# Kernel optimization log

Measured on AMD Instinct MI355X. Metric: run time of the kernel, lower is better.

## Reference

```python
import jax, jax.numpy as jnp
import numpy as np

B, N, DIM = 16, 1024, 512
H, DH = 8, 64
INNER = H * DH            # 512
FF = 4 * DIM              # 2048
CIN = 2 * DIM             # conv inner dim = dim*expansion_factor = 1024
K = 31                    # depthwise kernel size
MAXPOS = 512
EPS = 1e-5


def layernorm(x, g, b):
    mu = jnp.mean(x, axis=-1, keepdims=True)
    var = jnp.mean(jnp.square(x - mu), axis=-1, keepdims=True)
    return (x - mu) * jax.lax.rsqrt(var + EPS) * g + b


def swish(x):
    return x * jax.nn.sigmoid(x)


def feed_forward(x, w1, b1, w2, b2):
    h = swish(x @ w1 + b1)
    return h @ w2 + b2


def setup_inputs() -> dict:
    key = jax.random.key(0)
    ks = jax.random.split(key, 16)
    s = 0.02
    w = lambda k, shape: (jax.random.normal(k, shape, jnp.float32) * s)
    inp = {
        "x": jax.random.normal(ks[0], (B, N, DIM), jnp.float32),
        # FF1
        "ff1_ln_g": jnp.ones((DIM,), jnp.float32), "ff1_ln_b": jnp.zeros((DIM,), jnp.float32),
        "ff1_w1": w(ks[1], (DIM, FF)), "ff1_b1": jnp.zeros((FF,), jnp.float32),
        "ff1_w2": w(ks[2], (FF, DIM)), "ff1_b2": jnp.zeros((DIM,), jnp.float32),
        # Attention (PreNorm)
        "attn_ln_g": jnp.ones((DIM,), jnp.float32), "attn_ln_b": jnp.zeros((DIM,), jnp.float32),
        "wq": w(ks[3], (DIM, INNER)),
        "wkv": w(ks[4], (DIM, 2 * INNER)),
        "wo": w(ks[5], (INNER, DIM)), "bo": jnp.zeros((DIM,), jnp.float32),
        "rel_emb": w(ks[6], (2 * MAXPOS + 1, DH)),
        # Conv module
        "conv_ln_g": jnp.ones((DIM,), jnp.float32), "conv_ln_b": jnp.zeros((DIM,), jnp.float32),
        "conv1_w": w(ks[7], (DIM, 2 * CIN)), "conv1_b": jnp.zeros((2 * CIN,), jnp.float32),
        "dw_w": w(ks[8], (CIN, 1, K)), "dw_b": jnp.zeros((CIN,), jnp.float32),
        "conv2_w": w(ks[9], (CIN, DIM)), "conv2_b": jnp.zeros((DIM,), jnp.float32),
        # FF2
        "ff2_ln_g": jnp.ones((DIM,), jnp.float32), "ff2_ln_b": jnp.zeros((DIM,), jnp.float32),
        "ff2_w1": w(ks[10], (DIM, FF)), "ff2_b1": jnp.zeros((FF,), jnp.float32),
        "ff2_w2": w(ks[11], (FF, DIM)), "ff2_b2": jnp.zeros((DIM,), jnp.float32),
        # post norm
        "post_ln_g": jnp.ones((DIM,), jnp.float32), "post_ln_b": jnp.zeros((DIM,), jnp.float32),
    }
    return inp


def attention(x, wq, wkv, wo, bo, rel_emb):
    b, n, _ = x.shape
    scale = DH ** -0.5
    q = (x @ wq).reshape(b, n, H, DH).transpose(0, 2, 1, 3)   # b h n d
    kv = x @ wkv
    k = kv[..., :INNER].reshape(b, n, H, DH).transpose(0, 2, 1, 3)
    v = kv[..., INNER:].reshape(b, n, H, DH).transpose(0, 2, 1, 3)
    dots = jnp.einsum("bhid,bhjd->bhij", q, k) * scale
    # relative positional bias via embedding lookup
    seq = jnp.arange(n)
    dist = jnp.clip(seq[:, None] - seq[None, :], -MAXPOS, MAXPOS) + MAXPOS  # [n, n]
    rel = jnp.take(rel_emb, dist, axis=0)                      # [n, n, d]
    pos = jnp.einsum("bhnd,njd->bhnj", q, rel) * scale
    attn = jax.nn.softmax(dots + pos, axis=-1)
    out = jnp.einsum("bhij,bhjd->bhid", attn, v)
    out = out.transpose(0, 2, 1, 3).reshape(b, n, INNER)
    return out @ wo + bo


def conv_module(x, ln_g, ln_b, conv1_w, conv1_b, dw_w, dw_b, conv2_w, conv2_b):
    h = layernorm(x, ln_g, ln_b)                               # [b, n, dim]
    h = h @ conv1_w + conv1_b                                  # pointwise conv -> [b, n, 2*CIN]
    a, g = h[..., :CIN], h[..., CIN:]
    h = a * jax.nn.sigmoid(g)                                  # GLU (channel dim)
    hc = h.transpose(0, 2, 1)                                  # [b, CIN, n]
    hc = jnp.pad(hc, ((0, 0), (0, 0), (K - 1, 0)))             # causal left pad
    hc = jax.lax.conv_general_dilated(
        hc, dw_w, window_strides=(1,), padding="VALID",
        feature_group_count=CIN, dimension_numbers=("NCH", "OIH", "NCH"),
    ) + dw_b[None, :, None]
    h = hc.transpose(0, 2, 1)                                  # [b, n, CIN]
    h = swish(h)
    return h @ conv2_w + conv2_b


def reference(x, ff1_ln_g, ff1_ln_b, ff1_w1, ff1_b1, ff1_w2, ff1_b2,
              attn_ln_g, attn_ln_b, wq, wkv, wo, bo, rel_emb,
              conv_ln_g, conv_ln_b, conv1_w, conv1_b, dw_w, dw_b, conv2_w, conv2_b,
              ff2_ln_g, ff2_ln_b, ff2_w1, ff2_b1, ff2_w2, ff2_b2,
              post_ln_g, post_ln_b):
    x = 0.5 * feed_forward(layernorm(x, ff1_ln_g, ff1_ln_b), ff1_w1, ff1_b1, ff1_w2, ff1_b2) + x
    x = attention(layernorm(x, attn_ln_g, attn_ln_b), wq, wkv, wo, bo, rel_emb) + x
    x = conv_module(x, conv_ln_g, conv_ln_b, conv1_w, conv1_b, dw_w, dw_b, conv2_w, conv2_b) + x
    x = 0.5 * feed_forward(layernorm(x, ff2_ln_g, ff2_ln_b), ff2_w1, ff2_b1, ff2_w2, ff2_b2) + x
    return layernorm(x, post_ln_g, post_ln_b)
```

## Files before the change

kernel.cpp:

```cpp
#include <hip/hip_runtime.h>


#define BN 16384

typedef unsigned short u16;
typedef __attribute__((ext_vector_type(8))) __bf16 bf16x8;
typedef __attribute__((ext_vector_type(4))) float f32x4;
typedef __attribute__((ext_vector_type(8))) unsigned short u16x8;

__device__ __forceinline__ float sigf(float x) { return 1.f / (1.f + __expf(-x)); }
__device__ __forceinline__ u16 f2bf(float f) {
  unsigned int u = __float_as_uint(f);
  u += 0x7FFF + ((u >> 16) & 1);
  return (u16)(u >> 16);
}
__device__ __forceinline__ float bf2f(u16 u) {
  return __uint_as_float(((unsigned int)u) << 16);
}
__device__ __forceinline__ void gl_lds16(const void* g, void* lds) {
  __builtin_amdgcn_global_load_lds(
      (const __attribute__((address_space(1))) unsigned int*)g,
      (__attribute__((address_space(3))) unsigned int*)lds, 16, 0, 0);
}

__global__ __launch_bounds__(256) void ln_kernel(const float* __restrict__ in,
    const float* __restrict__ g, const float* __restrict__ b,
    u16* outb, float* outf) {
  const int row = blockIdx.x;
  const int t = threadIdx.x;
  const float2 v = ((const float2*)(in + (size_t)row * 512))[t];
  float s = v.x + v.y;
  float sq = v.x * v.x + v.y * v.y;
#pragma unroll
  for (int o = 32; o > 0; o >>= 1) {
    s += __shfl_down(s, o);
    sq += __shfl_down(sq, o);
  }
  __shared__ float ss[4], ssq[4];
  if ((t & 63) == 0) { ss[t >> 6] = s; ssq[t >> 6] = sq; }
  __syncthreads();
  s = ss[0] + ss[1] + ss[2] + ss[3];
  sq = ssq[0] + ssq[1] + ssq[2] + ssq[3];
  const float mu = s * (1.f / 512.f);
  const float var = fmaxf(sq * (1.f / 512.f) - mu * mu, 0.f);
  const float rstd = rsqrtf(var + 1e-5f);
  const float2 gg = ((const float2*)g)[t];
  const float2 bb = ((const float2*)b)[t];
  float ox = (v.x - mu) * rstd * gg.x + bb.x;
  float oy = (v.y - mu) * rstd * gg.y + bb.y;
  if (outf) {
    float2 o2 = {ox, oy};
    ((float2*)(outf + (size_t)row * 512))[t] = o2;
  } else {
    ushort2 u2 = {f2bf(ox), f2bf(oy)};
    ((ushort2*)(outb + (size_t)row * 512))[t] = u2;
  }
}

__global__ __launch_bounds__(256) void wtrans(const float* __restrict__ W,
                                              u16* __restrict__ WT, int K, int N) {
  const int n0 = blockIdx.x * 32, k0 = blockIdx.y * 32;
  const int t = threadIdx.x;
  const int tx = t & 31, ty = t >> 5;
  __shared__ float T[32][33];
#pragma unroll
  for (int i = 0; i < 4; ++i)
    T[tx][ty + 8 * i] = W[(size_t)(k0 + ty + 8 * i) * N + n0 + tx];
  __syncthreads();
#pragma unroll
  for (int i = 0; i < 4; ++i)
    WT[(size_t)(n0 + ty + 8 * i) * K + k0 + tx] = f2bf(T[ty + 8 * i][tx]);
}

__global__ __launch_bounds__(256) void cvt_bf16(const float* __restrict__ in,
                                                u16* __restrict__ out, int n) {
  const int i = blockIdx.x * 256 + threadIdx.x;
  if (i < n) out[i] = f2bf(in[i]);
}

__global__ __launch_bounds__(256) void gemm_bf16(const u16* __restrict__ A,
    const u16* __restrict__ WT, const float* __restrict__ bias,
    const float* res, float* Cf, u16* Cb, u16* VTout, int K, int N, int ldc,
    float alpha, int act) {
  __shared__ __align__(16) u16 Ast[128 * 32];
  __shared__ __align__(16) u16 Bst[128 * 32];
  const int t = threadIdx.x;
  int bx = blockIdx.x, by = blockIdx.y;
  {
    const int nx = gridDim.x;
    const int lin = bx + nx * by;
    const int xcd = lin & 7;
    const int s = lin >> 3;
    const int ny8 = gridDim.y >> 3;
    const int sy = s / nx;
    by = xcd * ny8 + sy;
    bx = s - sy * nx;
  }
  const int n0 = bx * 128;
  const int m0 = by * 128;
  const int w = t >> 6;
  const int lc = t & 15, lq = (t >> 4) & 3;
  const int wy = w >> 1, wx = w & 1;
  f32x4 acc[4][4];
#pragma unroll
  for (int i = 0; i < 4; ++i)
#pragma unroll
    for (int j = 0; j < 4; ++j)
#pragma unroll
      for (int r = 0; r < 4; ++r) acc[i][j][r] = 0.f;

  for (int kt = 0; kt < K; kt += 32) {
#pragma unroll
    for (int s = 0; s < 2; ++s) {
      const int f = t + 256 * s;
      gl_lds16(&A[(size_t)(m0 + (f >> 2)) * K + kt + (f & 3) * 8], &Ast[f * 8]);
      gl_lds16(&WT[(size_t)(n0 + (f >> 2)) * K + kt + (f & 3) * 8], &Bst[f * 8]);
    }
    __syncthreads();
    bf16x8 bfr[4];
#pragma unroll
    for (int j = 0; j < 4; ++j)
      bfr[j] = *(const bf16x8*)&Bst[(wx * 64 + j * 16 + lc) * 32 + lq * 8];
#pragma unroll
    for (int i = 0; i < 4; ++i) {
      const bf16x8 af = *(const bf16x8*)&Ast[(wy * 64 + i * 16 + lc) * 32 + lq * 8];
#pragma unroll
      for (int j = 0; j < 4; ++j)
        acc[i][j] = __builtin_amdgcn_mfma_f32_16x16x32_bf16(af, bfr[j], acc[i][j], 0, 0, 0);
    }
    __syncthreads();
  }

#pragma unroll
  for (int j = 0; j < 4; ++j) {
    const int col = n0 + wx * 64 + j * 16 + lc;
    const float bj = bias ? bias[col] : 0.f;
    const bool vtc = (VTout != nullptr) && (col >= 512);
#pragma unroll
    for (int i = 0; i < 4; ++i) {
      const int row0 = m0 + wy * 64 + i * 16 + lq * 4;
      float v4[4];
#pragma unroll
      for (int r = 0; r < 4; ++r) {
        float v = acc[i][j][r] + bj;
        if (act) v = v * sigf(v);
        v *= alpha;
        if (res) v += res[(size_t)(row0 + r) * ldc + col];
        v4[r] = v;
      }
      if (vtc) {
        const int cm = col - 512;
        const int hh = cm >> 6, dd = cm & 63;
        const int bb = row0 >> 10, nl = row0 & 1023;
        ushort4 o4 = {f2bf(v4[0]), f2bf(v4[1]), f2bf(v4[2]), f2bf(v4[3])};
        *(ushort4*)&VTout[((size_t)((bb * 8 + hh) * 64 + dd)) * 1024 + nl] = o4;
      } else {
#pragma unroll
        for (int r = 0; r < 4; ++r) {
          const size_t off = (size_t)(row0 + r) * ldc + col;
          if (Cf) Cf[off] = v4[r];
          else Cb[off] = f2bf(v4[r]);
        }
      }
    }
  }
}

__global__ __launch_bounds__(256) void attn_mfma(const u16* __restrict__ QKV,
    const u16* __restrict__ Vt, const u16* __restrict__ Rb, u16* __restrict__ O) {
  const int lin = blockIdx.x;
  const int hb = lin & 127;
  const int n0 = (lin >> 7) * 64;
  const int h = hb & 7, b = hb >> 3;
  const int t = threadIdx.x;
  const int w = t >> 6;
  const int lc = t & 15, lq = (t >> 4) & 3;

  __shared__ __align__(16) u16 Ks[2][64 * 64];
  __shared__ __align__(16) u16 Vs[2][64 * 64];
  __shared__ __align__(16) u16 SP[64 * 72];

  bf16x8 qf[2];
  {
    const size_t qrow = (size_t)(b * 1024 + n0 + w * 16 + lc) * 1536 + h * 64;
    qf[0] = *(const bf16x8*)&QKV[qrow + lq * 8];
    qf[1] = *(const bf16x8*)&QKV[qrow + 32 + lq * 8];
  }

  const u16* Kg = QKV + (size_t)b * 1024 * 1536 + 512 + h * 64;
  const u16* Vg = Vt + (size_t)(b * 8 + h) * 64 * 1024;

  const int srow = t >> 3;
  const int scb0 = ((t & 7) ^ (srow & 7)) * 8;
  const int srow1 = (t + 256) >> 3;
  const int scb1 = (((t + 256) & 7) ^ (srow1 & 7)) * 8;

  gl_lds16(&Kg[(size_t)srow * 1536 + scb0], &Ks[0][t * 8]);
  gl_lds16(&Vg[(size_t)srow * 1024 + scb0], &Vs[0][t * 8]);
  gl_lds16(&Kg[(size_t)srow1 * 1536 + scb1], &Ks[0][(t + 256) * 8]);
  gl_lds16(&Vg[(size_t)srow1 * 1024 + scb1], &Vs[0][(t + 256) * 8]);

  float l_r[4] = {0.f, 0.f, 0.f, 0.f};
  f32x4 o[4];
#pragma unroll
  for (int dt = 0; dt < 4; ++dt)
#pragma unroll
    for (int r = 0; r < 4; ++r) o[dt][r] = 0.f;

  const int swz0 = (lq ^ (lc & 7)) * 8;
  const int swz1 = ((4 + lq) ^ (lc & 7)) * 8;

  int buf = 0;
  for (int jt = 0; jt < 16; ++jt) {
    const int j0 = jt * 64;
    __syncthreads();

    if (jt < 15) {
      const int j1 = j0 + 64;
      gl_lds16(&Kg[(size_t)(j1 + srow) * 1536 + scb0], &Ks[buf ^ 1][t * 8]);
      gl_lds16(&Vg[(size_t)srow * 1024 + j1 + scb0], &Vs[buf ^ 1][t * 8]);
      gl_lds16(&Kg[(size_t)(j1 + srow1) * 1536 + scb1], &Ks[buf ^ 1][(t + 256) * 8]);
      gl_lds16(&Vg[(size_t)srow1 * 1024 + j1 + scb1], &Vs[buf ^ 1][(t + 256) * 8]);
    }

    f32x4 qk[4], pa[5];
#pragma unroll
    for (int j = 0; j < 4; ++j)
#pragma unroll
      for (int r = 0; r < 4; ++r) qk[j][r] = 0.f;
#pragma unroll
    for (int rtl = 0; rtl < 5; ++rtl)
#pragma unroll
      for (int r = 0; r < 4; ++r) pa[rtl][r] = 0.f;

    const int base = n0 - j0 - 63;
    const u16* rp[5];
#pragma unroll
    for (int rtl = 0; rtl < 5; ++rtl) {
      int p = base + (w + rtl) * 16 + lc;
      p = (p < -512 ? -512 : (p > 512 ? 512 : p)) + 512;
      rp[rtl] = Rb + (size_t)p * 64 + lq * 8;
    }

#pragma unroll
    for (int ks = 0; ks < 2; ++ks) {
      const int koff = ks ? swz1 : swz0;
      bf16x8 rfr[5];
#pragma unroll
      for (int rtl = 0; rtl < 5; ++rtl)
        rfr[rtl] = *(const bf16x8*)&rp[rtl][ks * 32];
#pragma unroll
      for (int j = 0; j < 4; ++j) {
        const bf16x8 bf = *(const bf16x8*)&Ks[buf][(j * 16 + lc) * 64 + koff];
        qk[j] = __builtin_amdgcn_mfma_f32_16x16x32_bf16(qf[ks], bf, qk[j], 0, 0, 0);
      }
#pragma unroll
      for (int rtl = 0; rtl < 5; ++rtl)
        pa[rtl] = __builtin_amdgcn_mfma_f32_16x16x32_bf16(qf[ks], rfr[rtl], pa[rtl], 0, 0, 0);
    }

#pragma unroll
    for (int rtl = 0; rtl < 5; ++rtl) {
      const int didx = (w + rtl) * 16 + lc;
#pragma unroll
      for (int r = 0; r < 4; ++r) {
        const int qr = w * 16 + lq * 4 + r;
        const int jc = qr - didx + 63;
        if ((unsigned)jc < 64u) SP[qr * 72 + jc] = f2bf(pa[rtl][r]);
      }
    }

#pragma unroll
    for (int r = 0; r < 4; ++r) {
      const int qr = w * 16 + lq * 4 + r;
#pragma unroll
      for (int ti = 0; ti < 4; ++ti) {
        const int a = qr * 72 + ti * 16 + lc;
        const float e = exp2f(qk[ti][r] + bf2f(SP[a]));
        SP[a] = f2bf(e);
        l_r[r] += e;
      }
    }

#pragma unroll
    for (int ks = 0; ks < 2; ++ks) {
      const bf16x8 af = *(const bf16x8*)&SP[(w * 16 + lc) * 72 + ks * 32 + lq * 8];
      const int koff = ks ? swz1 : swz0;
#pragma unroll
      for (int dt = 0; dt < 4; ++dt) {
        const bf16x8 bf = *(const bf16x8*)&Vs[buf][(dt * 16 + lc) * 64 + koff];
        o[dt] = __builtin_amdgcn_mfma_f32_16x16x32_bf16(af, bf, o[dt], 0, 0, 0);
      }
    }
    buf ^= 1;
  }

#pragma unroll
  for (int r = 0; r < 4; ++r) {
#pragma unroll
    for (int msk = 1; msk < 16; msk <<= 1) l_r[r] += __shfl_xor(l_r[r], msk);
  }

#pragma unroll
  for (int r = 0; r < 4; ++r) {
    const float inv = 1.f / l_r[r];
    const size_t row = (size_t)(b * 1024 + n0 + w * 16 + lq * 4 + r);
#pragma unroll
    for (int dt = 0; dt < 4; ++dt)
      O[row * 512 + h * 64 + dt * 16 + lc] = f2bf(o[dt][r] * inv);
  }
}

__global__ __launch_bounds__(256) void glu_kernel(const u16* __restrict__ in,
                                                  u16* __restrict__ out) {
  const size_t m = blockIdx.x;
  const int c4 = threadIdx.x * 4;
  const ushort4 a4 = *(const ushort4*)&in[m * 2048 + c4];
  const ushort4 g4 = *(const ushort4*)&in[m * 2048 + 1024 + c4];
  ushort4 o4;
  o4.x = f2bf(bf2f(a4.x) * sigf(bf2f(g4.x)));
  o4.y = f2bf(bf2f(a4.y) * sigf(bf2f(g4.y)));
  o4.z = f2bf(bf2f(a4.z) * sigf(bf2f(g4.z)));
  o4.w = f2bf(bf2f(a4.w) * sigf(bf2f(g4.w)));
  *(ushort4*)&out[m * 1024 + c4] = o4;
}

__global__ __launch_bounds__(256) void dwconv_kernel(const u16* __restrict__ in,
    const float* __restrict__ w, const float* __restrict__ bias,
    u16* __restrict__ out) {
  const int n0 = blockIdx.x * 64;
  const int c0 = blockIdx.y * 64;
  const int b = blockIdx.z;
  const int t = threadIdx.x;
  __shared__ float hs[94][64];
  __shared__ float wsh[31][64];
  const int c = t & 63;
  const int g = t >> 6;
  for (int r = g; r < 94; r += 4) {
    const int n = n0 - 30 + r;
    hs[r][c] = (n >= 0) ? bf2f(in[(size_t)(b * 1024 + n) * 1024 + c0 + c]) : 0.f;
  }
  for (int idx = t; idx < 31 * 64; idx += 256) {
    const int tap = idx >> 6, cc = idx & 63;
    wsh[tap][cc] = w[(size_t)(c0 + cc) * 31 + tap];
  }
  __syncthreads();
  float wr[31];
#pragma unroll
  for (int k = 0; k < 31; ++k) wr[k] = wsh[k][c];
  const float bsv = bias[c0 + c];
  float win[46];
  const int rbase = g * 16;
#pragma unroll
  for (int k = 0; k < 46; ++k) win[k] = hs[rbase + k][c];
#pragma unroll
  for (int i = 0; i < 16; ++i) {
    float acc = bsv;
#pragma unroll
    for (int k = 0; k < 31; ++k) acc += wr[k] * win[i + k];
    acc = acc * sigf(acc);
    out[(size_t)(b * 1024 + n0 + rbase + i) * 1024 + c0 + c] = f2bf(acc);
  }
}

extern "C" void kernel_launch(void* const* d_in, const int* in_sizes, int n_in,
                              void* d_out, int out_size, void* d_ws, size_t ws_size,
                              hipStream_t stream) {
  const float* x        = (const float*)d_in[0];
  const float* ff1_ln_g = (const float*)d_in[1];
  const float* ff1_ln_b = (const float*)d_in[2];
  const float* ff1_w1   = (const float*)d_in[3];
  const float* ff1_b1   = (const float*)d_in[4];
  const float* ff1_w2   = (const float*)d_in[5];
  const float* ff1_b2   = (const float*)d_in[6];
  const float* attn_ln_g= (const float*)d_in[7];
  const float* attn_ln_b= (const float*)d_in[8];
  const float* wq       = (const float*)d_in[9];
  const float* wkv      = (const float*)d_in[10];
  const float* wo       = (const float*)d_in[11];
  const float* bo       = (const float*)d_in[12];
  const float* rel_emb  = (const float*)d_in[13];
  const float* conv_ln_g= (const float*)d_in[14];
  const float* conv_ln_b= (const float*)d_in[15];
  const float* conv1_w  = (const float*)d_in[16];
  const float* conv1_b  = (const float*)d_in[17];
  const float* dw_w     = (const float*)d_in[18];
  const float* dw_b     = (const float*)d_in[19];
  const float* conv2_w  = (const float*)d_in[20];
  const float* conv2_b  = (const float*)d_in[21];
  const float* ff2_ln_g = (const float*)d_in[22];
  const float* ff2_ln_b = (const float*)d_in[23];
  const float* ff2_w1   = (const float*)d_in[24];
  const float* ff2_b1   = (const float*)d_in[25];
  const float* ff2_w2   = (const float*)d_in[26];
  const float* ff2_b2   = (const float*)d_in[27];
  const float* post_ln_g= (const float*)d_in[28];
  const float* post_ln_b= (const float*)d_in[29];

  float* XRES = (float*)d_out;
  u16* ws = (u16*)d_ws;
  u16* LNB  = ws;
  u16* HID  = LNB + (size_t)BN * 512;
  u16* QKVB = HID + (size_t)BN * 2048;
  u16* VT   = QKVB + (size_t)BN * 1536;
  u16* GLUB = QKVB;
  u16* DWB  = HID;
  u16* WTp = VT + (size_t)8192 * 1024;
  u16* wt_ff1w1 = WTp;                 WTp += (size_t)2048 * 512;
  u16* wt_ff1w2 = WTp;                 WTp += (size_t)512 * 2048;
  u16* wt_qkv   = WTp;                 WTp += (size_t)1536 * 512;
  u16* wt_wo    = WTp;                 WTp += (size_t)512 * 512;
  u16* wt_conv1 = WTp;                 WTp += (size_t)2048 * 512;
  u16* wt_conv2 = WTp;                 WTp += (size_t)512 * 1024;
  u16* wt_ff2w1 = WTp;                 WTp += (size_t)2048 * 512;
  u16* wt_ff2w2 = WTp;                 WTp += (size_t)512 * 2048;
  u16* RELB     = WTp;

  const dim3 blk(256);
  const float SC = 0.125f * 1.44269504f;

  wtrans<<<dim3(64, 16), blk, 0, stream>>>(ff1_w1, wt_ff1w1, 512, 2048);
  wtrans<<<dim3(16, 64), blk, 0, stream>>>(ff1_w2, wt_ff1w2, 2048, 512);
  wtrans<<<dim3(16, 16), blk, 0, stream>>>(wq, wt_qkv, 512, 512);
  wtrans<<<dim3(32, 16), blk, 0, stream>>>(wkv, wt_qkv + (size_t)512 * 512, 512, 1024);
  wtrans<<<dim3(16, 16), blk, 0, stream>>>(wo, wt_wo, 512, 512);
  wtrans<<<dim3(64, 16), blk, 0, stream>>>(conv1_w, wt_conv1, 512, 2048);
  wtrans<<<dim3(16, 32), blk, 0, stream>>>(conv2_w, wt_conv2, 1024, 512);
  wtrans<<<dim3(64, 16), blk, 0, stream>>>(ff2_w1, wt_ff2w1, 512, 2048);
  wtrans<<<dim3(16, 64), blk, 0, stream>>>(ff2_w2, wt_ff2w2, 2048, 512);
  cvt_bf16<<<257, blk, 0, stream>>>(rel_emb, RELB, 1025 * 64);

  ln_kernel<<<BN, blk, 0, stream>>>(x, ff1_ln_g, ff1_ln_b, LNB, nullptr);
  gemm_bf16<<<dim3(16, 128), blk, 0, stream>>>(LNB, wt_ff1w1, ff1_b1, nullptr,
                                               nullptr, HID, nullptr, 512, 2048, 2048, 1.f, 1);
  gemm_bf16<<<dim3(4, 128), blk, 0, stream>>>(HID, wt_ff1w2, ff1_b2, x,
                                              XRES, nullptr, nullptr, 2048, 512, 512, 0.5f, 0);

  ln_kernel<<<BN, blk, 0, stream>>>(XRES, attn_ln_g, attn_ln_b, LNB, nullptr);
  gemm_bf16<<<dim3(4, 128), blk, 0, stream>>>(LNB, wt_qkv, nullptr, nullptr,
                                              nullptr, QKVB, nullptr, 512, 512, 1536, SC, 0);
  gemm_bf16<<<dim3(8, 128), blk, 0, stream>>>(LNB, wt_qkv + (size_t)512 * 512,
                                              nullptr, nullptr, nullptr, QKVB + 512,
                                              VT, 512, 1024, 1536, 1.f, 0);
  attn_mfma<<<dim3(2048), blk, 0, stream>>>(QKVB, VT, RELB, LNB);
  gemm_bf16<<<dim3(4, 128), blk, 0, stream>>>(LNB, wt_wo, bo, XRES,
                                              XRES, nullptr, nullptr, 512, 512, 512, 1.f, 0);

  ln_kernel<<<BN, blk, 0, stream>>>(XRES, conv_ln_g, conv_ln_b, LNB, nullptr);
  gemm_bf16<<<dim3(16, 128), blk, 0, stream>>>(LNB, wt_conv1, conv1_b, nullptr,
                                               nullptr, HID, nullptr, 512, 2048, 2048, 1.f, 0);
  glu_kernel<<<BN, blk, 0, stream>>>(HID, GLUB);
  dwconv_kernel<<<dim3(16, 16, 16), blk, 0, stream>>>(GLUB, dw_w, dw_b, DWB);
  gemm_bf16<<<dim3(4, 128), blk, 0, stream>>>(DWB, wt_conv2, conv2_b, XRES,
                                              XRES, nullptr, nullptr, 1024, 512, 512, 1.f, 0);

  ln_kernel<<<BN, blk, 0, stream>>>(XRES, ff2_ln_g, ff2_ln_b, LNB, nullptr);
  gemm_bf16<<<dim3(16, 128), blk, 0, stream>>>(LNB, wt_ff2w1, ff2_b1, nullptr,
                                               nullptr, HID, nullptr, 512, 2048, 2048, 1.f, 1);
  gemm_bf16<<<dim3(4, 128), blk, 0, stream>>>(HID, wt_ff2w2, ff2_b2, XRES,
                                              XRES, nullptr, nullptr, 2048, 512, 512, 0.5f, 0);

  ln_kernel<<<BN, blk, 0, stream>>>(XRES, post_ln_g, post_ln_b, nullptr, XRES);
}
```

Before: 956.8 us.

## Share K/V tiles across two query groups per attention block

The attention kernel now launches 512-thread blocks covering 128 query rows (two 64-row groups of four waves each) instead of 256-thread blocks covering 64 rows. Each double-buffered K/V tile staged in LDS is reused by both groups, halving K/V global-to-LDS traffic per query, and each thread now issues one async load per tile instead of two. The cost is a larger score/probability scratch buffer and bigger blocks, which may change occupancy and make barrier stalls more expensive.

```diff
diff --git a/kernel.cpp b/kernel.cpp
--- a/kernel.cpp
+++ b/kernel.cpp
@@ -166,23 +166,25 @@
   }
 }
 
-__global__ __launch_bounds__(256) void attn_mfma(const u16* __restrict__ QKV,
+__global__ __launch_bounds__(512) void attn_mfma(const u16* __restrict__ QKV,
     const u16* __restrict__ Vt, const u16* __restrict__ Rb, u16* __restrict__ O) {
   const int lin = blockIdx.x;
   const int hb = lin & 127;
-  const int n0 = (lin >> 7) * 64;
+  const int N0 = (lin >> 7) * 128;
   const int h = hb & 7, b = hb >> 3;
   const int t = threadIdx.x;
   const int w = t >> 6;
+  const int wl = w & 3;
+  const int n0 = N0 + (w >> 2) * 64;
   const int lc = t & 15, lq = (t >> 4) & 3;
 
   __shared__ __align__(16) u16 Ks[2][64 * 64];
   __shared__ __align__(16) u16 Vs[2][64 * 64];
-  __shared__ __align__(16) u16 SP[64 * 72];
+  __shared__ __align__(16) u16 SP[128 * 72];
 
   bf16x8 qf[2];
   {
-    const size_t qrow = (size_t)(b * 1024 + n0 + w * 16 + lc) * 1536 + h * 64;
+    const size_t qrow = (size_t)(b * 1024 + n0 + wl * 16 + lc) * 1536 + h * 64;
     qf[0] = *(const bf16x8*)&QKV[qrow + lq * 8];
     qf[1] = *(const bf16x8*)&QKV[qrow + 32 + lq * 8];
   }
@@ -191,14 +193,10 @@
   const u16* Vg = Vt + (size_t)(b * 8 + h) * 64 * 1024;
 
   const int srow = t >> 3;
-  const int scb0 = ((t & 7) ^ (srow & 7)) * 8;
-  const int srow1 = (t + 256) >> 3;
-  const int scb1 = (((t + 256) & 7) ^ (srow1 & 7)) * 8;
-
-  gl_lds16(&Kg[(size_t)srow * 1536 + scb0], &Ks[0][t * 8]);
-  gl_lds16(&Vg[(size_t)srow * 1024 + scb0], &Vs[0][t * 8]);
-  gl_lds16(&Kg[(size_t)srow1 * 1536 + scb1], &Ks[0][(t + 256) * 8]);
-  gl_lds16(&Vg[(size_t)srow1 * 1024 + scb1], &Vs[0][(t + 256) * 8]);
+  const int scb = ((t & 7) ^ (srow & 7)) * 8;
+
+  gl_lds16(&Kg[(size_t)srow * 1536 + scb], &Ks[0][t * 8]);
+  gl_lds16(&Vg[(size_t)srow * 1024 + scb], &Vs[0][t * 8]);
 
   float l_r[4] = {0.f, 0.f, 0.f, 0.f};
   f32x4 o[4];
@@ -217,10 +215,8 @@
 
     if (jt < 15) {
       const int j1 = j0 + 64;
-      gl_lds16(&Kg[(size_t)(j1 + srow) * 1536 + scb0], &Ks[buf ^ 1][t * 8]);
-      gl_lds16(&Vg[(size_t)srow * 1024 + j1 + scb0], &Vs[buf ^ 1][t * 8]);
-      gl_lds16(&Kg[(size_t)(j1 + srow1) * 1536 + scb1], &Ks[buf ^ 1][(t + 256) * 8]);
-      gl_lds16(&Vg[(size_t)srow1 * 1024 + j1 + scb1], &Vs[buf ^ 1][(t + 256) * 8]);
+      gl_lds16(&Kg[(size_t)(j1 + srow) * 1536 + scb], &Ks[buf ^ 1][t * 8]);
+      gl_lds16(&Vg[(size_t)srow * 1024 + j1 + scb], &Vs[buf ^ 1][t * 8]);
     }
 
     f32x4 qk[4], pa[5];
@@ -237,7 +233,7 @@
     const u16* rp[5];
 #pragma unroll
     for (int rtl = 0; rtl < 5; ++rtl) {
-      int p = base + (w + rtl) * 16 + lc;
+      int p = base + (wl + rtl) * 16 + lc;
       p = (p < -512 ? -512 : (p > 512 ? 512 : p)) + 512;
       rp[rtl] = Rb + (size_t)p * 64 + lq * 8;
     }
@@ -261,12 +257,12 @@
 
 #pragma unroll
     for (int rtl = 0; rtl < 5; ++rtl) {
-      const int didx = (w + rtl) * 16 + lc;
+      const int didx = (wl + rtl) * 16 + lc;
 #pragma unroll
       for (int r = 0; r < 4; ++r) {
-        const int qr = w * 16 + lq * 4 + r;
-        const int jc = qr - didx + 63;
-        if ((unsigned)jc < 64u) SP[qr * 72 + jc] = f2bf(pa[rtl][r]);
+        const int qlocal = wl * 16 + lq * 4 + r;
+        const int jc = qlocal - didx + 63;
+        if ((unsigned)jc < 64u) SP[(w * 16 + lq * 4 + r) * 72 + jc] = f2bf(pa[rtl][r]);
       }
     }
 
@@ -304,7 +300,7 @@
 #pragma unroll
   for (int r = 0; r < 4; ++r) {
     const float inv = 1.f / l_r[r];
-    const size_t row = (size_t)(b * 1024 + n0 + w * 16 + lq * 4 + r);
+    const size_t row = (size_t)(b * 1024 + N0 + w * 16 + lq * 4 + r);
 #pragma unroll
     for (int dt = 0; dt < 4; ++dt)
       O[row * 512 + h * 64 + dt * 16 + lc] = f2bf(o[dt][r] * inv);
@@ -442,7 +438,7 @@
   gemm_bf16<<<dim3(8, 128), blk, 0, stream>>>(LNB, wt_qkv + (size_t)512 * 512,
                                               nullptr, nullptr, nullptr, QKVB + 512,
                                               VT, 512, 1024, 1536, 1.f, 0);
-  attn_mfma<<<dim3(2048), blk, 0, stream>>>(QKVB, VT, RELB, LNB);
+  attn_mfma<<<dim3(1024), dim3(512), 0, stream>>>(QKVB, VT, RELB, LNB);
   gemm_bf16<<<dim3(4, 128), blk, 0, stream>>>(LNB, wt_wo, bo, XRES,
                                               XRES, nullptr, nullptr, 512, 512, 512, 1.f, 0);
 
```

Result: slower. 1.028 ms (+7.5%).

## Deepen GEMM K-tile to 64 with XOR-swizzled LDS and fuse Q/KV projections

Applied to the files above, without the earlier changes.

The bf16 GEMM now stages a 64-wide K slice per iteration instead of 32, which halves the number of barrier pairs per tile. It stores the LDS tiles with an XOR swizzle on 16-byte chunks so MFMA fragment reads avoid bank conflicts. The separate Q and KV projection GEMMs become a single launch over all 1536 output columns, with per-column alpha scaling (via qn) and a parameterized V-transpose start column (vt0). LDS use doubles to 32 KB per block, which may reduce occupancy.

```diff
diff --git a/kernel.cpp b/kernel.cpp
--- a/kernel.cpp
+++ b/kernel.cpp
@@ -81,9 +81,9 @@
 __global__ __launch_bounds__(256) void gemm_bf16(const u16* __restrict__ A,
     const u16* __restrict__ WT, const float* __restrict__ bias,
     const float* res, float* Cf, u16* Cb, u16* VTout, int K, int N, int ldc,
-    float alpha, int act) {
-  __shared__ __align__(16) u16 Ast[128 * 32];
-  __shared__ __align__(16) u16 Bst[128 * 32];
+    float alpha, int act, int qn, int vt0) {
+  __shared__ __align__(16) u16 Ast[128 * 64];
+  __shared__ __align__(16) u16 Bst[128 * 64];
   const int t = threadIdx.x;
   int bx = blockIdx.x, by = blockIdx.y;
   {
@@ -109,24 +109,33 @@
 #pragma unroll
       for (int r = 0; r < 4; ++r) acc[i][j][r] = 0.f;
 
-  for (int kt = 0; kt < K; kt += 32) {
-#pragma unroll
-    for (int s = 0; s < 2; ++s) {
+  const int koff0 = (lq ^ (lc & 7)) * 8;
+  const int koff1 = ((4 + lq) ^ (lc & 7)) * 8;
+
+  for (int kt = 0; kt < K; kt += 64) {
+#pragma unroll
+    for (int s = 0; s < 4; ++s) {
       const int f = t + 256 * s;
-      gl_lds16(&A[(size_t)(m0 + (f >> 2)) * K + kt + (f & 3) * 8], &Ast[f * 8]);
-      gl_lds16(&WT[(size_t)(n0 + (f >> 2)) * K + kt + (f & 3) * 8], &Bst[f * 8]);
+      const int fr = f >> 3;
+      const int fc = (f & 7) ^ (fr & 7);
+      gl_lds16(&A[(size_t)(m0 + fr) * K + kt + fc * 8], &Ast[f * 8]);
+      gl_lds16(&WT[(size_t)(n0 + fr) * K + kt + fc * 8], &Bst[f * 8]);
     }
     __syncthreads();
-    bf16x8 bfr[4];
-#pragma unroll
-    for (int j = 0; j < 4; ++j)
-      bfr[j] = *(const bf16x8*)&Bst[(wx * 64 + j * 16 + lc) * 32 + lq * 8];
-#pragma unroll
-    for (int i = 0; i < 4; ++i) {
-      const bf16x8 af = *(const bf16x8*)&Ast[(wy * 64 + i * 16 + lc) * 32 + lq * 8];
+#pragma unroll
+    for (int kk = 0; kk < 2; ++kk) {
+      const int koff = kk ? koff1 : koff0;
+      bf16x8 bfr[4];
 #pragma unroll
       for (int j = 0; j < 4; ++j)
-        acc[i][j] = __builtin_amdgcn_mfma_f32_16x16x32_bf16(af, bfr[j], acc[i][j], 0, 0, 0);
+        bfr[j] = *(const bf16x8*)&Bst[(wx * 64 + j * 16 + lc) * 64 + koff];
+#pragma unroll
+      for (int i = 0; i < 4; ++i) {
+        const bf16x8 af = *(const bf16x8*)&Ast[(wy * 64 + i * 16 + lc) * 64 + koff];
+#pragma unroll
+        for (int j = 0; j < 4; ++j)
+          acc[i][j] = __builtin_amdgcn_mfma_f32_16x16x32_bf16(af, bfr[j], acc[i][j], 0, 0, 0);
+      }
     }
     __syncthreads();
   }
@@ -135,7 +144,8 @@
   for (int j = 0; j < 4; ++j) {
     const int col = n0 + wx * 64 + j * 16 + lc;
     const float bj = bias ? bias[col] : 0.f;
-    const bool vtc = (VTout != nullptr) && (col >= 512);
+    const float al = (col < qn) ? alpha : 1.f;
+    const bool vtc = (VTout != nullptr) && (col >= vt0);
 #pragma unroll
     for (int i = 0; i < 4; ++i) {
       const int row0 = m0 + wy * 64 + i * 16 + lq * 4;
@@ -144,12 +154,12 @@
       for (int r = 0; r < 4; ++r) {
         float v = acc[i][j][r] + bj;
         if (act) v = v * sigf(v);
-        v *= alpha;
+        v *= al;
         if (res) v += res[(size_t)(row0 + r) * ldc + col];
         v4[r] = v;
       }
       if (vtc) {
-        const int cm = col - 512;
+        const int cm = col - vt0;
         const int hh = cm >> 6, dd = cm & 63;
         const int bb = row0 >> 10, nl = row0 & 1023;
         ushort4 o4 = {f2bf(v4[0]), f2bf(v4[1]), f2bf(v4[2]), f2bf(v4[3])};
@@ -432,33 +442,30 @@
 
   ln_kernel<<<BN, blk, 0, stream>>>(x, ff1_ln_g, ff1_ln_b, LNB, nullptr);
   gemm_bf16<<<dim3(16, 128), blk, 0, stream>>>(LNB, wt_ff1w1, ff1_b1, nullptr,
-                                               nullptr, HID, nullptr, 512, 2048, 2048, 1.f, 1);
+                                               nullptr, HID, nullptr, 512, 2048, 2048, 1.f, 1, 2048, 0);
   gemm_bf16<<<dim3(4, 128), blk, 0, stream>>>(HID, wt_ff1w2, ff1_b2, x,
-                                              XRES, nullptr, nullptr, 2048, 512, 512, 0.5f, 0);
+                                              XRES, nullptr, nullptr, 2048, 512, 512, 0.5f, 0, 512, 0);
 
   ln_kernel<<<BN, blk, 0, stream>>>(XRES, attn_ln_g, attn_ln_b, LNB, nullptr);
-  gemm_bf16<<<dim3(4, 128), blk, 0, stream>>>(LNB, wt_qkv, nullptr, nullptr,
-                                              nullptr, QKVB, nullptr, 512, 512, 1536, SC, 0);
-  gemm_bf16<<<dim3(8, 128), blk, 0, stream>>>(LNB, wt_qkv + (size_t)512 * 512,
-                                              nullptr, nullptr, nullptr, QKVB + 512,
-                                              VT, 512, 1024, 1536, 1.f, 0);
+  gemm_bf16<<<dim3(12, 128), blk, 0, stream>>>(LNB, wt_qkv, nullptr, nullptr,
+                                               nullptr, QKVB, VT, 512, 1536, 1536, SC, 0, 512, 1024);
   attn_mfma<<<dim3(2048), blk, 0, stream>>>(QKVB, VT, RELB, LNB);
   gemm_bf16<<<dim3(4, 128), blk, 0, stream>>>(LNB, wt_wo, bo, XRES,
-                                              XRES, nullptr, nullptr, 512, 512, 512, 1.f, 0);
+                                              XRES, nullptr, nullptr, 512, 512, 512, 1.f, 0, 512, 0);
 
   ln_kernel<<<BN, blk, 0, stream>>>(XRES, conv_ln_g, conv_ln_b, LNB, nullptr);
   gemm_bf16<<<dim3(16, 128), blk, 0, stream>>>(LNB, wt_conv1, conv1_b, nullptr,
-                                               nullptr, HID, nullptr, 512, 2048, 2048, 1.f, 0);
+                                               nullptr, HID, nullptr, 512, 2048, 2048, 1.f, 0, 2048, 0);
   glu_kernel<<<BN, blk, 0, stream>>>(HID, GLUB);
   dwconv_kernel<<<dim3(16, 16, 16), blk, 0, stream>>>(GLUB, dw_w, dw_b, DWB);
   gemm_bf16<<<dim3(4, 128), blk, 0, stream>>>(DWB, wt_conv2, conv2_b, XRES,
-                                              XRES, nullptr, nullptr, 1024, 512, 512, 1.f, 0);
+                                              XRES, nullptr, nullptr, 1024, 512, 512, 1.f, 0, 512, 0);
 
   ln_kernel<<<BN, blk, 0, stream>>>(XRES, ff2_ln_g, ff2_ln_b, LNB, nullptr);
   gemm_bf16<<<dim3(16, 128), blk, 0, stream>>>(LNB, wt_ff2w1, ff2_b1, nullptr,
-                                               nullptr, HID, nullptr, 512, 2048, 2048, 1.f, 1);
+                                               nullptr, HID, nullptr, 512, 2048, 2048, 1.f, 1, 2048, 0);
   gemm_bf16<<<dim3(4, 128), blk, 0, stream>>>(HID, wt_ff2w2, ff2_b2, XRES,
-                                              XRES, nullptr, nullptr, 2048, 512, 512, 0.5f, 0);
+                                              XRES, nullptr, nullptr, 2048, 512, 512, 0.5f, 0, 512, 0);
 
   ln_kernel<<<BN, blk, 0, stream>>>(XRES, post_ln_g, post_ln_b, nullptr, XRES);
 }
```

New measurement: 920.8 us. 1.04x faster.
